# Kernel tuning notes

Measured on AMD Instinct MI355X. Metric: run time of the kernel, lower is better.

## Reference

```python
import jax, jax.numpy as jnp
import numpy as np

FEAT_SIZE, HIDDEN_SIZE, ATT_SIZE = 2048, 1024, 512
BATCH, FEAT_NUM = 64, 512


def setup_inputs() -> dict:
    key = jax.random.key(0)
    ks = jax.random.split(key, 8)
    s = lambda fan_in: 1.0 / np.sqrt(fan_in)
    return {
        "feats": jax.random.normal(ks[0], (BATCH, FEAT_NUM, FEAT_SIZE), jnp.float32),
        "key": jax.random.normal(ks[1], (BATCH, HIDDEN_SIZE), jnp.float32),
        "wh_w": jax.random.uniform(ks[2], (ATT_SIZE, HIDDEN_SIZE), jnp.float32, -s(HIDDEN_SIZE), s(HIDDEN_SIZE)),
        "wh_b": jax.random.uniform(ks[3], (ATT_SIZE,), jnp.float32, -s(HIDDEN_SIZE), s(HIDDEN_SIZE)),
        "wv_w": jax.random.uniform(ks[4], (ATT_SIZE, FEAT_SIZE), jnp.float32, -s(FEAT_SIZE), s(FEAT_SIZE)),
        "wv_b": jax.random.uniform(ks[5], (ATT_SIZE,), jnp.float32, -s(FEAT_SIZE), s(FEAT_SIZE)),
        "wa_w": jax.random.uniform(ks[6], (1, ATT_SIZE), jnp.float32, -s(ATT_SIZE), s(ATT_SIZE)),
    }


def reference(feats, key, wh_w, wh_b, wv_w, wv_b, wa_w):
    # v = wv(feats): (B, N, A)
    v = jnp.einsum('bnf,af->bna', feats, wv_w) + wv_b
    # h = wh(key): (B, A), broadcast-added over feat_num
    h = key @ wh_w.T + wh_b
    inputs = h[:, None, :] + v                       # (B, N, A)
    scores = jnp.einsum('bna,a->bn', jnp.tanh(inputs), wa_w[0])  # (B, N)
    alpha = jax.nn.softmax(scores, axis=1)           # (B, N)
    att_feats = jnp.einsum('bn,bnf->bf', alpha, feats)  # (B, F)
    return (att_feats, alpha)
```

## Files before the change

### kernel.cpp

```cpp
#include <hip/hip_runtime.h>
#include <hip/hip_bf16.h>

#define FEATSZ 2048
#define HIDSZ  1024
#define ATTSZ  512
#define BATCH  64
#define FEATN  512

typedef float  f32x4  __attribute__((ext_vector_type(4)));
typedef __bf16 bf16x8 __attribute__((ext_vector_type(8)));

__device__ __forceinline__ unsigned short f2bf(float f) {
    union { float f; unsigned int u; } x; x.f = f;
    unsigned int u = x.u;
    return (unsigned short)((u + 0x7fffu + ((u >> 16) & 1u)) >> 16);
}

__global__ void k_h(const float* __restrict__ key, const float* __restrict__ wh_w,
                    const float* __restrict__ wh_b, float* __restrict__ h) {
    const int b = blockIdx.y;
    const int ac = blockIdx.x;
    const int t = threadIdx.x;
    const int lane = t & 63, wv = t >> 6;
    float k16[16];
    const float* kb = key + b * HIDSZ;
#pragma unroll
    for (int j = 0; j < 16; ++j) k16[j] = kb[lane + 64 * j];
#pragma unroll 1
    for (int i = 0; i < 16; ++i) {
        int a = ac * 64 + wv * 16 + i;
        const float* wr = wh_w + (size_t)a * HIDSZ;
        float s = 0.f;
#pragma unroll
        for (int j = 0; j < 16; ++j) s += k16[j] * wr[lane + 64 * j];
#pragma unroll
        for (int d = 32; d; d >>= 1) s += __shfl_xor(s, d);
        if (lane == 0) h[b * ATTSZ + a] = s + wh_b[a];
    }
}

__global__ void k_wvcvt(const float* __restrict__ wv_w, unsigned short* __restrict__ wvb) {
    int idx = blockIdx.x * 256 + threadIdx.x;
    int a = idx >> 11, k = idx & 2047;
    int CF = a >> 4, c = a & 15, ks = k >> 5, kin = k & 31;
    int lane = c + ((kin >> 3) << 4);
    int dst = ((ks * 32 + CF) * 64 + lane) * 8 + (kin & 7);
    wvb[dst] = f2bf(wv_w[idx]);
}

__global__ __launch_bounds__(512, 4) void k_scores(
        const float* __restrict__ feats, const unsigned short* __restrict__ wvb,
        const float* __restrict__ h, const float* __restrict__ wv_b,
        const float* __restrict__ wa, float* __restrict__ scores) {
    __shared__ __align__(16) char smem[65536];
    const int t = threadIdx.x;
    const int lane = t & 63, w = t >> 6;
    const int m0 = blockIdx.x * 64;
    const int b = m0 >> 9;

    const char* fbase = (const char*)feats;
    unsigned int goff[4];
    unsigned int ldst[4];
#pragma unroll
    for (int s = 0; s < 4; ++s) {
        int q = w * 256 + s * 64 + lane;
        int r = q >> 5;
        int c = (q & 31) ^ (r & 7);
        goff[s] = (unsigned int)(((m0 + r) * 2048 + c * 4) * 4);
        ldst[s] = (unsigned int)(w * 4096 + s * 1024);
    }

    const int A0 = (lane & 15) * 512 + ((((lane >> 4) * 2)    ) ^ (lane & 7)) * 16;
    const int A1 = (lane & 15) * 512 + ((((lane >> 4) * 2) | 1) ^ (lane & 7)) * 16;

    auto stage = [&](int bufc, int it) {
#pragma unroll
        for (int s = 0; s < 4; ++s)
            __builtin_amdgcn_global_load_lds(
                (const __attribute__((address_space(1))) void*)(fbase + goff[s] + it * 512),
                (__attribute__((address_space(3))) void*)(smem + bufc * 32768 + ldst[s]),
                16, 0, 0);
    };

    const unsigned short* wb = wvb + w * 2048 + lane * 8;
    bf16x8 bn[4];
    auto loadB = [&](int kk) {
#pragma unroll
        for (int cf = 0; cf < 4; ++cf) bn[cf] = *(const bf16x8*)(wb + kk * 16384 + cf * 512);
    };

    f32x4 acc[4][4];
#pragma unroll
    for (int m = 0; m < 4; ++m)
#pragma unroll
        for (int cf = 0; cf < 4; ++cf) acc[m][cf] = (f32x4)0.0f;

    stage(0, 0);
    loadB(0);
    __syncthreads();

    auto kiter = [&](int it, int bufc) {
        if (it < 15) stage(bufc ^ 1, it + 1);
#pragma unroll
        for (int ks = 0; ks < 4; ++ks) {
            bf16x8 bc[4];
#pragma unroll
            for (int cf = 0; cf < 4; ++cf) bc[cf] = bn[cf];
            int kk = it * 4 + ks + 1; if (kk > 63) kk = 63;
            loadB(kk);
#pragma unroll
            for (int m = 0; m < 4; ++m) {
                const char* ap = (const char*)smem + bufc * 32768 + m * 8192 + ks * 128;
                f32x4 fa = *(const f32x4*)(ap + A0);
                f32x4 fb = *(const f32x4*)(ap + A1);
                unsigned int q0, q1, q2, q3;
                asm("v_cvt_pk_bf16_f32 %0, %1, %2" : "=v"(q0) : "v"(fa.x), "v"(fa.y));
                asm("v_cvt_pk_bf16_f32 %0, %1, %2" : "=v"(q1) : "v"(fa.z), "v"(fa.w));
                asm("v_cvt_pk_bf16_f32 %0, %1, %2" : "=v"(q2) : "v"(fb.x), "v"(fb.y));
                asm("v_cvt_pk_bf16_f32 %0, %1, %2" : "=v"(q3) : "v"(fb.z), "v"(fb.w));
                union { unsigned int u[4]; bf16x8 v; } af;
                af.u[0] = q0; af.u[1] = q1; af.u[2] = q2; af.u[3] = q3;
#pragma unroll
                for (int cf = 0; cf < 4; ++cf)
                    acc[m][cf] = __builtin_amdgcn_mfma_f32_16x16x32_bf16(af.v, bc[cf], acc[m][cf], 0, 0, 0);
            }
        }
        __syncthreads();
    };

#pragma unroll 1
    for (int it2 = 0; it2 < 8; ++it2) {
        kiter(it2 * 2, 0);
        kiter(it2 * 2 + 1, 1);
    }

    const int c16 = lane & 15, q4 = lane >> 4;
    float hreg[4], wreg[4];
#pragma unroll
    for (int cf = 0; cf < 4; ++cf) {
        int a = w * 64 + cf * 16 + c16;
        hreg[cf] = h[b * ATTSZ + a] + wv_b[a];
        wreg[cf] = wa[a];
    }
    float p[4][4];
#pragma unroll
    for (int m = 0; m < 4; ++m)
#pragma unroll
        for (int j = 0; j < 4; ++j) p[m][j] = 0.f;
#pragma unroll
    for (int m = 0; m < 4; ++m)
#pragma unroll
        for (int cf = 0; cf < 4; ++cf) {
#pragma unroll
            for (int j = 0; j < 4; ++j)
                p[m][j] += tanhf(acc[m][cf][j] + hreg[cf]) * wreg[cf];
        }
#pragma unroll
    for (int m = 0; m < 4; ++m)
#pragma unroll
        for (int j = 0; j < 4; ++j) {
            float v = p[m][j];
            v += __shfl_xor(v, 1); v += __shfl_xor(v, 2);
            v += __shfl_xor(v, 4); v += __shfl_xor(v, 8);
            p[m][j] = v;
        }
    float* scp = (float*)smem;
    if (c16 == 0) {
#pragma unroll
        for (int m = 0; m < 4; ++m)
#pragma unroll
            for (int j = 0; j < 4; ++j)
                scp[w * 64 + m * 16 + q4 * 4 + j] = p[m][j];
    }
    __syncthreads();
    if (t < 64) {
        float s = 0.f;
#pragma unroll
        for (int ww = 0; ww < 8; ++ww) s += scp[ww * 64 + t];
        scores[m0 + t] = s;
    }
}

__global__ void k_softmax(const float* __restrict__ scores, float* __restrict__ alpha) {
    __shared__ float red[16];
    const int b = blockIdx.x, t = threadIdx.x;
    const int lane = t & 63, w = t >> 6;
    float s = scores[b * FEATN + t];
    float m = s;
#pragma unroll
    for (int d = 32; d; d >>= 1) m = fmaxf(m, __shfl_xor(m, d));
    if (lane == 0) red[w] = m;
    __syncthreads();
    if (t == 0) {
        float mm = red[0];
        for (int i = 1; i < 8; ++i) mm = fmaxf(mm, red[i]);
        red[8] = mm;
    }
    __syncthreads();
    float e = __expf(s - red[8]);
    float sum = e;
#pragma unroll
    for (int d = 32; d; d >>= 1) sum += __shfl_xor(sum, d);
    if (lane == 0) red[w] = sum;
    __syncthreads();
    if (t == 0) {
        float ss = 0.f;
        for (int i = 0; i < 8; ++i) ss += red[i];
        red[9] = 1.0f / ss;
    }
    __syncthreads();
    alpha[b * FEATN + t] = e * red[9];
}

__global__ void k_att_part(const float* __restrict__ feats, const float* __restrict__ alpha,
                           float* __restrict__ part) {
    const int b = blockIdx.x, fc = blockIdx.y, ns = blockIdx.z, t = threadIdx.x;
    const int f0 = fc * 1024 + t * 4;
    const float* fp = feats + (size_t)(b * FEATN + ns * 128) * FEATSZ + f0;
    const float* al = alpha + b * FEATN + ns * 128;
    float4 acc = {0.f, 0.f, 0.f, 0.f};
#pragma unroll 4
    for (int i = 0; i < 128; ++i) {
        float a = al[i];
        float4 v = *(const float4*)(fp + (size_t)i * FEATSZ);
        acc.x += a * v.x; acc.y += a * v.y; acc.z += a * v.z; acc.w += a * v.w;
    }
    *(float4*)(part + ((size_t)ns * BATCH + b) * FEATSZ + f0) = acc;
}

__global__ void k_att_red(const float* __restrict__ part, float* __restrict__ out) {
    const int idx = (blockIdx.x * 256 + threadIdx.x) * 4;
    float4 s = *(const float4*)(part + idx);
#pragma unroll
    for (int z = 1; z < 4; ++z) {
        float4 v = *(const float4*)(part + (size_t)z * (BATCH * FEATSZ) + idx);
        s.x += v.x; s.y += v.y; s.z += v.z; s.w += v.w;
    }
    *(float4*)(out + idx) = s;
}

extern "C" void kernel_launch(void* const* d_in, const int* in_sizes, int n_in,
                              void* d_out, int out_size, void* d_ws, size_t ws_size,
                              hipStream_t stream) {
    const float* feats = (const float*)d_in[0];
    const float* key   = (const float*)d_in[1];
    const float* wh_w  = (const float*)d_in[2];
    const float* wh_b  = (const float*)d_in[3];
    const float* wv_w  = (const float*)d_in[4];
    const float* wv_b  = (const float*)d_in[5];
    const float* wa_w  = (const float*)d_in[6];

    float* out_att   = (float*)d_out;
    float* out_alpha = out_att + BATCH * FEATSZ;

    char* ws = (char*)d_ws;
    float* h              = (float*)(ws);
    float* scores         = (float*)(ws + 131072);
    unsigned short* wvb   = (unsigned short*)(ws + 262144);
    float* part           = (float*)(ws + 262144);

    hipLaunchKernelGGL(k_h,        dim3(8, 64),    dim3(256), 0, stream, key, wh_w, wh_b, h);
    hipLaunchKernelGGL(k_wvcvt,    dim3(4096),     dim3(256), 0, stream, wv_w, wvb);
    hipLaunchKernelGGL(k_scores,   dim3(512),      dim3(512), 0, stream, feats, wvb, h, wv_b, wa_w, scores);
    hipLaunchKernelGGL(k_softmax,  dim3(64),       dim3(512), 0, stream, scores, out_alpha);
    hipLaunchKernelGGL(k_att_part, dim3(64, 2, 4), dim3(256), 0, stream, feats, out_alpha, part);
    hipLaunchKernelGGL(k_att_red,  dim3(128),      dim3(256), 0, stream, part, out_att);
}
```

Baseline: 174.1 us.

## Enlarge scores GEMM tile to 128 rows with half-depth K stages

The scores kernel now processes 128 feature rows per block instead of 64, halving the grid to 256 blocks. Each wave reuses every loaded weight fragment across 8 row tiles, which halves the weight traffic from global or L2 per row. The K stage is cut to 64 elements so the double-buffered LDS footprint stays the same, with 32 iterations replacing 16. Register use doubles for accumulators and launch bounds drop to 2 blocks per CU. On a chip with 256 CUs this leaves roughly one block per CU and less latency hiding, and the fp32-to-bf16 conversion now uses plain casts instead of inline asm.

```diff
diff --git a/kernel.cpp b/kernel.cpp
--- a/kernel.cpp
+++ b/kernel.cpp
@@ -48,90 +48,97 @@
     wvb[dst] = f2bf(wv_w[idx]);
 }
 
-__global__ __launch_bounds__(512, 4) void k_scores(
+__global__ __launch_bounds__(512, 2) void k_scores(
         const float* __restrict__ feats, const unsigned short* __restrict__ wvb,
         const float* __restrict__ h, const float* __restrict__ wv_b,
         const float* __restrict__ wa, float* __restrict__ scores) {
     __shared__ __align__(16) char smem[65536];
     const int t = threadIdx.x;
     const int lane = t & 63, w = t >> 6;
-    const int m0 = blockIdx.x * 64;
-    const int b = m0 >> 9;
+    const int m0 = blockIdx.x * 128;
+    const int b = blockIdx.x >> 2;
 
     const char* fbase = (const char*)feats;
-    unsigned int goff[4];
-    unsigned int ldst[4];
+    unsigned int goff[4], ldst[4];
 #pragma unroll
     for (int s = 0; s < 4; ++s) {
         int q = w * 256 + s * 64 + lane;
-        int r = q >> 5;
-        int c = (q & 31) ^ (r & 7);
+        int r = q >> 4, c = (q & 15) ^ (r & 7);
         goff[s] = (unsigned int)(((m0 + r) * 2048 + c * 4) * 4);
         ldst[s] = (unsigned int)(w * 4096 + s * 1024);
     }
-
-    const int A0 = (lane & 15) * 512 + ((((lane >> 4) * 2)    ) ^ (lane & 7)) * 16;
-    const int A1 = (lane & 15) * 512 + ((((lane >> 4) * 2) | 1) ^ (lane & 7)) * 16;
-
-    auto stage = [&](int bufc, int it) {
+    auto stage = [&](int buf, int it) {
 #pragma unroll
         for (int s = 0; s < 4; ++s)
             __builtin_amdgcn_global_load_lds(
-                (const __attribute__((address_space(1))) void*)(fbase + goff[s] + it * 512),
-                (__attribute__((address_space(3))) void*)(smem + bufc * 32768 + ldst[s]),
+                (const __attribute__((address_space(1))) void*)(fbase + goff[s] + it * 256),
+                (__attribute__((address_space(3))) void*)(smem + buf * 32768 + ldst[s]),
                 16, 0, 0);
     };
 
-    const unsigned short* wb = wvb + w * 2048 + lane * 8;
-    bf16x8 bn[4];
-    auto loadB = [&](int kk) {
-#pragma unroll
-        for (int cf = 0; cf < 4; ++cf) bn[cf] = *(const bf16x8*)(wb + kk * 16384 + cf * 512);
-    };
-
-    f32x4 acc[4][4];
-#pragma unroll
-    for (int m = 0; m < 4; ++m)
+    const unsigned short* wb = wvb + lane * 8;
+    bf16x8 bnA[4], bnB[4];
+    auto loadBA = [&](int kk) {
+#pragma unroll
+        for (int cf = 0; cf < 4; ++cf) bnA[cf] = *(const bf16x8*)(wb + (kk * 32 + w * 4 + cf) * 512);
+    };
+    auto loadBB = [&](int kk) {
+#pragma unroll
+        for (int cf = 0; cf < 4; ++cf) bnB[cf] = *(const bf16x8*)(wb + (kk * 32 + w * 4 + cf) * 512);
+    };
+
+    const int sw = lane & 7, kq2 = (lane >> 4) * 2;
+    const int off0 = (lane & 15) * 256 + ((kq2    ) ^ sw) * 16;
+    const int off1 = (lane & 15) * 256 + ((kq2 | 1) ^ sw) * 16;
+
+    f32x4 acc[8][4];
+#pragma unroll
+    for (int m = 0; m < 8; ++m)
 #pragma unroll
         for (int cf = 0; cf < 4; ++cf) acc[m][cf] = (f32x4)0.0f;
 
     stage(0, 0);
-    loadB(0);
-    __syncthreads();
-
-    auto kiter = [&](int it, int bufc) {
-        if (it < 15) stage(bufc ^ 1, it + 1);
-#pragma unroll
-        for (int ks = 0; ks < 4; ++ks) {
-            bf16x8 bc[4];
-#pragma unroll
-            for (int cf = 0; cf < 4; ++cf) bc[cf] = bn[cf];
-            int kk = it * 4 + ks + 1; if (kk > 63) kk = 63;
-            loadB(kk);
-#pragma unroll
-            for (int m = 0; m < 4; ++m) {
-                const char* ap = (const char*)smem + bufc * 32768 + m * 8192 + ks * 128;
-                f32x4 fa = *(const f32x4*)(ap + A0);
-                f32x4 fb = *(const f32x4*)(ap + A1);
-                unsigned int q0, q1, q2, q3;
-                asm("v_cvt_pk_bf16_f32 %0, %1, %2" : "=v"(q0) : "v"(fa.x), "v"(fa.y));
-                asm("v_cvt_pk_bf16_f32 %0, %1, %2" : "=v"(q1) : "v"(fa.z), "v"(fa.w));
-                asm("v_cvt_pk_bf16_f32 %0, %1, %2" : "=v"(q2) : "v"(fb.x), "v"(fb.y));
-                asm("v_cvt_pk_bf16_f32 %0, %1, %2" : "=v"(q3) : "v"(fb.z), "v"(fb.w));
-                union { unsigned int u[4]; bf16x8 v; } af;
-                af.u[0] = q0; af.u[1] = q1; af.u[2] = q2; af.u[3] = q3;
-#pragma unroll
-                for (int cf = 0; cf < 4; ++cf)
-                    acc[m][cf] = __builtin_amdgcn_mfma_f32_16x16x32_bf16(af.v, bc[cf], acc[m][cf], 0, 0, 0);
-            }
+    loadBA(0);
+    __syncthreads();
+
+    auto domfmaA = [&](int buf, int ks) {
+#pragma unroll
+        for (int m = 0; m < 8; ++m) {
+            const char* ap = smem + buf * 32768 + m * 4096 + ks * 128;
+            f32x4 fa = *(const f32x4*)__builtin_assume_aligned(ap + off0, 16);
+            f32x4 fb = *(const f32x4*)__builtin_assume_aligned(ap + off1, 16);
+            bf16x8 af;
+            af[0] = (__bf16)fa[0]; af[1] = (__bf16)fa[1]; af[2] = (__bf16)fa[2]; af[3] = (__bf16)fa[3];
+            af[4] = (__bf16)fb[0]; af[5] = (__bf16)fb[1]; af[6] = (__bf16)fb[2]; af[7] = (__bf16)fb[3];
+#pragma unroll
+            for (int cf = 0; cf < 4; ++cf)
+                acc[m][cf] = __builtin_amdgcn_mfma_f32_16x16x32_bf16(af, bnA[cf], acc[m][cf], 0, 0, 0);
         }
+    };
+    auto domfmaB = [&](int buf, int ks) {
+#pragma unroll
+        for (int m = 0; m < 8; ++m) {
+            const char* ap = smem + buf * 32768 + m * 4096 + ks * 128;
+            f32x4 fa = *(const f32x4*)__builtin_assume_aligned(ap + off0, 16);
+            f32x4 fb = *(const f32x4*)__builtin_assume_aligned(ap + off1, 16);
+            bf16x8 af;
+            af[0] = (__bf16)fa[0]; af[1] = (__bf16)fa[1]; af[2] = (__bf16)fa[2]; af[3] = (__bf16)fa[3];
+            af[4] = (__bf16)fb[0]; af[5] = (__bf16)fb[1]; af[6] = (__bf16)fb[2]; af[7] = (__bf16)fb[3];
+#pragma unroll
+            for (int cf = 0; cf < 4; ++cf)
+                acc[m][cf] = __builtin_amdgcn_mfma_f32_16x16x32_bf16(af, bnB[cf], acc[m][cf], 0, 0, 0);
+        }
+    };
+
+#pragma unroll 1
+    for (int it = 0; it < 32; ++it) {
+        const int buf = it & 1;
+        if (it < 31) stage(buf ^ 1, it + 1);
+        loadBB(2 * it + 1);
+        domfmaA(buf, 0);
+        loadBA(2 * it + 2 > 63 ? 63 : 2 * it + 2);
+        domfmaB(buf, 1);
         __syncthreads();
-    };
-
-#pragma unroll 1
-    for (int it2 = 0; it2 < 8; ++it2) {
-        kiter(it2 * 2, 0);
-        kiter(it2 * 2 + 1, 1);
     }
 
     const int c16 = lane & 15, q4 = lane >> 4;
@@ -142,21 +149,20 @@
         hreg[cf] = h[b * ATTSZ + a] + wv_b[a];
         wreg[cf] = wa[a];
     }
-    float p[4][4];
-#pragma unroll
-    for (int m = 0; m < 4; ++m)
+    float p[8][4];
+#pragma unroll
+    for (int m = 0; m < 8; ++m)
 #pragma unroll
         for (int j = 0; j < 4; ++j) p[m][j] = 0.f;
 #pragma unroll
-    for (int m = 0; m < 4; ++m)
-#pragma unroll
-        for (int cf = 0; cf < 4; ++cf) {
+    for (int m = 0; m < 8; ++m)
+#pragma unroll
+        for (int cf = 0; cf < 4; ++cf)
 #pragma unroll
             for (int j = 0; j < 4; ++j)
                 p[m][j] += tanhf(acc[m][cf][j] + hreg[cf]) * wreg[cf];
-        }
-#pragma unroll
-    for (int m = 0; m < 4; ++m)
+#pragma unroll
+    for (int m = 0; m < 8; ++m)
 #pragma unroll
         for (int j = 0; j < 4; ++j) {
             float v = p[m][j];
@@ -167,16 +173,16 @@
     float* scp = (float*)smem;
     if (c16 == 0) {
 #pragma unroll
-        for (int m = 0; m < 4; ++m)
+        for (int m = 0; m < 8; ++m)
 #pragma unroll
             for (int j = 0; j < 4; ++j)
-                scp[w * 64 + m * 16 + q4 * 4 + j] = p[m][j];
-    }
-    __syncthreads();
-    if (t < 64) {
+                scp[w * 128 + m * 16 + q4 * 4 + j] = p[m][j];
+    }
+    __syncthreads();
+    if (t < 128) {
         float s = 0.f;
 #pragma unroll
-        for (int ww = 0; ww < 8; ++ww) s += scp[ww * 64 + t];
+        for (int ww = 0; ww < 8; ++ww) s += scp[ww * 128 + t];
         scores[m0 + t] = s;
     }
 }
@@ -261,7 +267,7 @@
 
     hipLaunchKernelGGL(k_h,        dim3(8, 64),    dim3(256), 0, stream, key, wh_w, wh_b, h);
     hipLaunchKernelGGL(k_wvcvt,    dim3(4096),     dim3(256), 0, stream, wv_w, wvb);
-    hipLaunchKernelGGL(k_scores,   dim3(512),      dim3(512), 0, stream, feats, wvb, h, wv_b, wa_w, scores);
+    hipLaunchKernelGGL(k_scores,   dim3(256),      dim3(512), 0, stream, feats, wvb, h, wv_b, wa_w, scores);
     hipLaunchKernelGGL(k_softmax,  dim3(64),       dim3(512), 0, stream, scores, out_alpha);
     hipLaunchKernelGGL(k_att_part, dim3(64, 2, 4), dim3(256), 0, stream, feats, out_alpha, part);
     hipLaunchKernelGGL(k_att_red,  dim3(128),      dim3(256), 0, stream, part, out_att);
```

Measured after the change: 164.1 us. 1.06x faster.

## Stage feats as bf16 in LDS via register prefetch with smaller K-tiles

Applied to the files above, without the earlier changes.

Replaces the direct global-to-LDS fp32 staging (64 KB of LDS, 128-wide K tiles) with a register-prefetched load. Each feats tile is converted to bf16 once before being written to a swizzled 16 KB double buffer, so the per-MFMA fp32-to-bf16 conversion and the large LDS footprint go away, which may allow more resident blocks. The K loop now runs 32 steps of 64, interleaving weight prefetch between two half-steps and raising wave priority around the MFMA bursts. The cost is a barrier every 64 K elements and global-load latency that is exposed through registers rather than async copies.

```diff
diff --git a/kernel.cpp b/kernel.cpp
--- a/kernel.cpp
+++ b/kernel.cpp
@@ -52,41 +52,34 @@
         const float* __restrict__ feats, const unsigned short* __restrict__ wvb,
         const float* __restrict__ h, const float* __restrict__ wv_b,
         const float* __restrict__ wa, float* __restrict__ scores) {
-    __shared__ __align__(16) char smem[65536];
+    __shared__ __align__(16) char smem[2][8192];
+    __shared__ float scp[8][64];
     const int t = threadIdx.x;
     const int lane = t & 63, w = t >> 6;
     const int m0 = blockIdx.x * 64;
-    const int b = m0 >> 9;
-
-    const char* fbase = (const char*)feats;
-    unsigned int goff[4];
-    unsigned int ldst[4];
-#pragma unroll
-    for (int s = 0; s < 4; ++s) {
-        int q = w * 256 + s * 64 + lane;
-        int r = q >> 5;
-        int c = (q & 31) ^ (r & 7);
-        goff[s] = (unsigned int)(((m0 + r) * 2048 + c * 4) * 4);
-        ldst[s] = (unsigned int)(w * 4096 + s * 1024);
-    }
-
-    const int A0 = (lane & 15) * 512 + ((((lane >> 4) * 2)    ) ^ (lane & 7)) * 16;
-    const int A1 = (lane & 15) * 512 + ((((lane >> 4) * 2) | 1) ^ (lane & 7)) * 16;
-
-    auto stage = [&](int bufc, int it) {
-#pragma unroll
-        for (int s = 0; s < 4; ++s)
-            __builtin_amdgcn_global_load_lds(
-                (const __attribute__((address_space(1))) void*)(fbase + goff[s] + it * 512),
-                (__attribute__((address_space(3))) void*)(smem + bufc * 32768 + ldst[s]),
-                16, 0, 0);
+    const int b = blockIdx.x >> 3;
+
+    const int sr = t >> 3, sc = t & 7;
+    const float* gsrc = feats + (size_t)(m0 + sr) * FEATSZ + sc * 8;
+    const int swoff = sr * 128 + ((sc ^ (sr & 7)) * 16);
+
+    auto stconv = [&](int buf, float4 s0, float4 s1) {
+        bf16x8 af;
+        af[0] = (__bf16)s0.x; af[1] = (__bf16)s0.y; af[2] = (__bf16)s0.z; af[3] = (__bf16)s0.w;
+        af[4] = (__bf16)s1.x; af[5] = (__bf16)s1.y; af[6] = (__bf16)s1.z; af[7] = (__bf16)s1.w;
+        *(bf16x8*)__builtin_assume_aligned(&smem[buf][swoff], 16) = af;
     };
 
-    const unsigned short* wb = wvb + w * 2048 + lane * 8;
-    bf16x8 bn[4];
-    auto loadB = [&](int kk) {
-#pragma unroll
-        for (int cf = 0; cf < 4; ++cf) bn[cf] = *(const bf16x8*)(wb + kk * 16384 + cf * 512);
+    const int fr = lane & 15, fq = lane >> 4;
+    const int ra0 = fr * 128 + (((0 + fq) ^ (fr & 7)) * 16);
+    const int ra1 = fr * 128 + (((4 + fq) ^ (fr & 7)) * 16);
+
+    const unsigned short* wb = wvb + lane * 8;
+    bf16x8 bnA[4];
+    auto loadBA = [&](int kk) {
+#pragma unroll
+        for (int cf = 0; cf < 4; ++cf)
+            bnA[cf] = *(const bf16x8*)(wb + (kk * 32 + w * 4 + cf) * 512);
     };
 
     f32x4 acc[4][4];
@@ -95,43 +88,61 @@
 #pragma unroll
         for (int cf = 0; cf < 4; ++cf) acc[m][cf] = (f32x4)0.0f;
 
-    stage(0, 0);
-    loadB(0);
-    __syncthreads();
-
-    auto kiter = [&](int it, int bufc) {
-        if (it < 15) stage(bufc ^ 1, it + 1);
-#pragma unroll
-        for (int ks = 0; ks < 4; ++ks) {
-            bf16x8 bc[4];
-#pragma unroll
-            for (int cf = 0; cf < 4; ++cf) bc[cf] = bn[cf];
-            int kk = it * 4 + ks + 1; if (kk > 63) kk = 63;
-            loadB(kk);
-#pragma unroll
-            for (int m = 0; m < 4; ++m) {
-                const char* ap = (const char*)smem + bufc * 32768 + m * 8192 + ks * 128;
-                f32x4 fa = *(const f32x4*)(ap + A0);
-                f32x4 fb = *(const f32x4*)(ap + A1);
-                unsigned int q0, q1, q2, q3;
-                asm("v_cvt_pk_bf16_f32 %0, %1, %2" : "=v"(q0) : "v"(fa.x), "v"(fa.y));
-                asm("v_cvt_pk_bf16_f32 %0, %1, %2" : "=v"(q1) : "v"(fa.z), "v"(fa.w));
-                asm("v_cvt_pk_bf16_f32 %0, %1, %2" : "=v"(q2) : "v"(fb.x), "v"(fb.y));
-                asm("v_cvt_pk_bf16_f32 %0, %1, %2" : "=v"(q3) : "v"(fb.z), "v"(fb.w));
-                union { unsigned int u[4]; bf16x8 v; } af;
-                af.u[0] = q0; af.u[1] = q1; af.u[2] = q2; af.u[3] = q3;
-#pragma unroll
-                for (int cf = 0; cf < 4; ++cf)
-                    acc[m][cf] = __builtin_amdgcn_mfma_f32_16x16x32_bf16(af.v, bc[cf], acc[m][cf], 0, 0, 0);
-            }
-        }
+    {
+        float4 s0 = *(const float4*)gsrc;
+        float4 s1 = *(const float4*)(gsrc + 4);
+        loadBA(0);
+        stconv(0, s0, s1);
+    }
+    __syncthreads();
+
+#pragma unroll 1
+    for (int it = 0; it < 32; ++it) {
+        const char* ab = &smem[it & 1][0];
+        bf16x8 bnB[4];
+#pragma unroll
+        for (int cf = 0; cf < 4; ++cf)
+            bnB[cf] = *(const bf16x8*)(wb + ((2 * it + 1) * 32 + w * 4 + cf) * 512);
+        float4 s0, s1;
+        if (it < 31) {
+            s0 = *(const float4*)(gsrc + (it + 1) * 64);
+            s1 = *(const float4*)(gsrc + (it + 1) * 64 + 4);
+        }
+        {
+            bf16x8 a0 = *(const bf16x8*)__builtin_assume_aligned(ab + 0 * 2048 + ra0, 16);
+            bf16x8 a1 = *(const bf16x8*)__builtin_assume_aligned(ab + 1 * 2048 + ra0, 16);
+            bf16x8 a2 = *(const bf16x8*)__builtin_assume_aligned(ab + 2 * 2048 + ra0, 16);
+            bf16x8 a3 = *(const bf16x8*)__builtin_assume_aligned(ab + 3 * 2048 + ra0, 16);
+            __builtin_amdgcn_s_setprio(1);
+#pragma unroll
+            for (int cf = 0; cf < 4; ++cf) acc[0][cf] = __builtin_amdgcn_mfma_f32_16x16x32_bf16(a0, bnA[cf], acc[0][cf], 0, 0, 0);
+#pragma unroll
+            for (int cf = 0; cf < 4; ++cf) acc[1][cf] = __builtin_amdgcn_mfma_f32_16x16x32_bf16(a1, bnA[cf], acc[1][cf], 0, 0, 0);
+#pragma unroll
+            for (int cf = 0; cf < 4; ++cf) acc[2][cf] = __builtin_amdgcn_mfma_f32_16x16x32_bf16(a2, bnA[cf], acc[2][cf], 0, 0, 0);
+#pragma unroll
+            for (int cf = 0; cf < 4; ++cf) acc[3][cf] = __builtin_amdgcn_mfma_f32_16x16x32_bf16(a3, bnA[cf], acc[3][cf], 0, 0, 0);
+            __builtin_amdgcn_s_setprio(0);
+        }
+        if (it < 31) loadBA(2 * it + 2);
+        {
+            bf16x8 a0 = *(const bf16x8*)__builtin_assume_aligned(ab + 0 * 2048 + ra1, 16);
+            bf16x8 a1 = *(const bf16x8*)__builtin_assume_aligned(ab + 1 * 2048 + ra1, 16);
+            bf16x8 a2 = *(const bf16x8*)__builtin_assume_aligned(ab + 2 * 2048 + ra1, 16);
+            bf16x8 a3 = *(const bf16x8*)__builtin_assume_aligned(ab + 3 * 2048 + ra1, 16);
+            __builtin_amdgcn_s_setprio(1);
+#pragma unroll
+            for (int cf = 0; cf < 4; ++cf) acc[0][cf] = __builtin_amdgcn_mfma_f32_16x16x32_bf16(a0, bnB[cf], acc[0][cf], 0, 0, 0);
+#pragma unroll
+            for (int cf = 0; cf < 4; ++cf) acc[1][cf] = __builtin_amdgcn_mfma_f32_16x16x32_bf16(a1, bnB[cf], acc[1][cf], 0, 0, 0);
+#pragma unroll
+            for (int cf = 0; cf < 4; ++cf) acc[2][cf] = __builtin_amdgcn_mfma_f32_16x16x32_bf16(a2, bnB[cf], acc[2][cf], 0, 0, 0);
+#pragma unroll
+            for (int cf = 0; cf < 4; ++cf) acc[3][cf] = __builtin_amdgcn_mfma_f32_16x16x32_bf16(a3, bnB[cf], acc[3][cf], 0, 0, 0);
+            __builtin_amdgcn_s_setprio(0);
+        }
+        if (it < 31) stconv((it + 1) & 1, s0, s1);
         __syncthreads();
-    };
-
-#pragma unroll 1
-    for (int it2 = 0; it2 < 8; ++it2) {
-        kiter(it2 * 2, 0);
-        kiter(it2 * 2 + 1, 1);
     }
 
     const int c16 = lane & 15, q4 = lane >> 4;
@@ -150,11 +161,10 @@
 #pragma unroll
     for (int m = 0; m < 4; ++m)
 #pragma unroll
-        for (int cf = 0; cf < 4; ++cf) {
+        for (int cf = 0; cf < 4; ++cf)
 #pragma unroll
             for (int j = 0; j < 4; ++j)
                 p[m][j] += tanhf(acc[m][cf][j] + hreg[cf]) * wreg[cf];
-        }
 #pragma unroll
     for (int m = 0; m < 4; ++m)
 #pragma unroll
@@ -164,19 +174,18 @@
             v += __shfl_xor(v, 4); v += __shfl_xor(v, 8);
             p[m][j] = v;
         }
-    float* scp = (float*)smem;
     if (c16 == 0) {
 #pragma unroll
         for (int m = 0; m < 4; ++m)
 #pragma unroll
             for (int j = 0; j < 4; ++j)
-                scp[w * 64 + m * 16 + q4 * 4 + j] = p[m][j];
+                scp[w][m * 16 + q4 * 4 + j] = p[m][j];
     }
     __syncthreads();
     if (t < 64) {
         float s = 0.f;
 #pragma unroll
-        for (int ww = 0; ww < 8; ++ww) s += scp[ww * 64 + t];
+        for (int ww = 0; ww < 8; ++ww) s += scp[ww][t];
         scores[m0 + t] = s;
     }
 }
```

New measurement: 188.3 us. +8.1%, slower.
